# Kernel tuning notes

Measured on AMD Instinct MI355X. Metric: run time of the kernel, lower is better.

## Reference

```python
import jax, jax.numpy as jnp
import numpy as np

B, S, F = 4, 2048, 128
H, D = 4, 128          # num_heads, hidden_dim
OUT = 128              # out_features
NEG_SLOPE = 0.01       # torch leaky_relu default


def setup_inputs() -> dict:
    key = jax.random.key(0)
    ks = jax.random.split(key, 8)
    h = jax.random.normal(ks[0], (B, S, F), dtype=jnp.float32)
    # bool mask, True = masked-out key position (as used by masked_fill_)
    mask = jax.random.randint(ks[1], (B, S), 0, 2).astype(jnp.bool_)
    # Linear params (torch Linear: y = x @ W.T + b), kaiming-ish scale
    W_w = jax.random.normal(ks[2], (H * D, F), dtype=jnp.float32) / np.sqrt(F)
    W_b = jnp.zeros((H * D,), dtype=jnp.float32)
    a_w = jax.random.normal(ks[3], (1, 2 * D), dtype=jnp.float32) / np.sqrt(2 * D)
    a_b = jnp.zeros((1,), dtype=jnp.float32)
    out_w = jax.random.normal(ks[4], (OUT, H * D), dtype=jnp.float32) / np.sqrt(H * D)
    out_b = jnp.zeros((OUT,), dtype=jnp.float32)
    return {"h": h, "mask": mask, "W_w": W_w, "W_b": W_b,
            "a_w": a_w, "a_b": a_b, "out_w": out_w, "out_b": out_b}


def reference(h, mask, W_w, W_b, a_w, a_b, out_w, out_b):
    # h: [B,S,F] -> per-head projection hp: [B,H,S,D]
    hp = (h @ W_w.T + W_b).reshape(B, S, H, D).transpose(0, 2, 1, 3)
    # Additive GAT score a([h_i, h_j]) splits into two rank-1 contributions:
    # score[b,n,i,j] = leaky_relu(a1 . h_i + a2 . h_j + b)  (same math as the
    # original full [B,H,S,S,2D] concat + Linear, without materializing it).
    a1, a2 = a_w[0, :D], a_w[0, D:]
    e1 = jnp.einsum('bhsd,d->bhs', hp, a1)  # query-side term
    e2 = jnp.einsum('bhsd,d->bhs', hp, a2)  # key-side term
    scores = jax.nn.leaky_relu(e1[..., :, None] + e2[..., None, :] + a_b[0],
                               negative_slope=NEG_SLOPE)  # [B,H,S,S]
    # mask broadcast to [B,1,1,S]: masks key positions
    scores = jnp.where(mask[:, None, None, :], -jnp.inf, scores)
    attn = jax.nn.softmax(scores, axis=-1)  # [B,H,S,S]
    ctx = jnp.einsum('bhij,bhjd->bhid', attn, hp)  # [B,H,S,D]
    ctx = ctx.transpose(0, 2, 1, 3).reshape(B, S, H * D)
    out = jax.nn.relu(ctx @ out_w.T + out_b)  # [B,S,OUT]
    return out, attn
```

## Files before the change

kernel.cpp:

```cpp
#include <hip/hip_runtime.h>
#include <hip/hip_bf16.h>

#define BB 4
#define SS 2048
#define FF 128
#define DD 128
#define HD 512
#define OUTD 128
#define BH 16
#define NSL 0.01f
#define NC 258
#define NCH 128
#define CHK 16

typedef __hip_bfloat16 bf16;
typedef short bf16x8 __attribute__((ext_vector_type(8)));
typedef float f32x4 __attribute__((ext_vector_type(4)));

constexpr size_t OFF_HPF = 0;
constexpr size_t OFF_E1  = OFF_HPF + (size_t)BB*SS*HD;
constexpr size_t OFF_E2  = OFF_E1 + (size_t)BH*SS;
constexpr size_t OFF_M2  = OFF_E2 + (size_t)BH*SS;
constexpr size_t OFF_U   = OFF_M2 + 64;
constexpr size_t OFF_V   = OFF_U + (size_t)BH*SS;
constexpr size_t OFF_DS  = OFF_V + (size_t)BH*SS;
constexpr size_t OFF_SIG = OFF_DS + (size_t)BH*SS;
constexpr size_t OFF_PL  = OFF_SIG + (size_t)BH*SS;
constexpr size_t OFF_CS  = OFF_PL + (size_t)BH*2049*NC;
constexpr size_t OFF_O   = OFF_CS + (size_t)BH*NCH*NC;
constexpr size_t OFF_TOT = OFF_O + (size_t)BH*NCH*NC;
constexpr size_t OFF_CTX = OFF_TOT + (size_t)BH*NC;

__device__ inline void load8_split(const float* __restrict__ p, bf16x8& hi, bf16x8& lo) {
  f32x4 x0 = *(const f32x4*)p;
  f32x4 x1 = *(const f32x4*)(p + 4);
#pragma unroll
  for (int e = 0; e < 8; ++e) {
    float x = (e < 4) ? x0[e] : x1[e - 4];
    __hip_bfloat16 hb = __float2bfloat16(x);
    float hf = __bfloat162float(hb);
    __hip_bfloat16 lb = __float2bfloat16(x - hf);
    hi[e] = (short)__bfloat16_as_ushort(hb);
    lo[e] = (short)__bfloat16_as_ushort(lb);
  }
}

__global__ __launch_bounds__(256) void k1_hp(const float* __restrict__ h, const float* __restrict__ Ww,
                                             const float* __restrict__ Wb, float* __restrict__ hpf) {
  int wid = threadIdx.x >> 6, lane = threadIdx.x & 63;
  int tile = blockIdx.x * 4 + wid;
  int mt = tile >> 5, nt = tile & 31;
  int s0 = mt * 16, n0 = nt * 16;
  int row = lane & 15, g = lane >> 4;
  const float* pa = h  + (size_t)(s0 + row) * FF + g * 8;
  const float* pb = Ww + (size_t)(n0 + row) * FF + g * 8;
  f32x4 acc = {0.f,0.f,0.f,0.f};
#pragma unroll
  for (int ks = 0; ks < 4; ++ks) {
    bf16x8 ah, al, bh_, bl;
    load8_split(pa + ks*32, ah, al);
    load8_split(pb + ks*32, bh_, bl);
    acc = __builtin_amdgcn_mfma_f32_16x16x32_bf16(ah, bh_, acc, 0, 0, 0);
    acc = __builtin_amdgcn_mfma_f32_16x16x32_bf16(ah, bl,  acc, 0, 0, 0);
    acc = __builtin_amdgcn_mfma_f32_16x16x32_bf16(al, bh_, acc, 0, 0, 0);
  }
  int col = lane & 15;
  float bias = Wb[n0 + col];
#pragma unroll
  for (int r = 0; r < 4; ++r) {
    int orow = g*4 + r;
    hpf[(size_t)(s0 + orow) * HD + n0 + col] = acc[r] + bias;
  }
}

__global__ __launch_bounds__(256) void k2_e(const float* __restrict__ hpf, const float* __restrict__ aw,
                                            float* __restrict__ e1, float* __restrict__ e2) {
  int wid = threadIdx.x >> 6, lane = threadIdx.x & 63;
  int gw = blockIdx.x * 4 + wid;
  int bh = gw >> 11, s = gw & 2047;
  int b = bh >> 2, hh = bh & 3;
  const float* rowp = hpf + (size_t)(b*SS + s) * HD + hh * DD;
  float a1a = aw[lane],      a1b = aw[lane + 64];
  float a2a = aw[DD + lane], a2b = aw[DD + lane + 64];
  float xa = rowp[lane], xb = rowp[lane + 64];
  float r1 = xa*a1a + xb*a1b;
  float r2 = xa*a2a + xb*a2b;
  for (int o = 32; o; o >>= 1) { r1 += __shfl_down(r1, o); r2 += __shfl_down(r2, o); }
  if (lane == 0) { e1[(size_t)bh*SS + s] = r1; e2[(size_t)bh*SS + s] = r2; }
}

__global__ __launch_bounds__(256) void k2b_uv(const float* __restrict__ e2, const int* __restrict__ mask,
                                              float* __restrict__ m2out, float* __restrict__ u, float* __restrict__ v) {
  int bh = blockIdx.x; int b = bh >> 2;
  __shared__ float red[256];
  float mx = -1e30f;
  for (int j = threadIdx.x; j < SS; j += 256) {
    float val = e2[(size_t)bh*SS + j];
    if (!mask[b*SS + j]) mx = fmaxf(mx, val);
  }
  red[threadIdx.x] = mx; __syncthreads();
  for (int st = 128; st; st >>= 1) {
    if (threadIdx.x < st) red[threadIdx.x] = fmaxf(red[threadIdx.x], red[threadIdx.x + st]);
    __syncthreads();
  }
  float m2 = red[0];
  if (threadIdx.x == 0) m2out[bh] = m2;
  for (int j = threadIdx.x; j < SS; j += 256) {
    float d = e2[(size_t)bh*SS + j] - m2;
    int mk = mask[b*SS + j];
    u[(size_t)bh*SS + j] = mk ? 0.f : expf(d);
    v[(size_t)bh*SS + j] = mk ? 0.f : expf(NSL * d);
  }
}

__global__ __launch_bounds__(1024) void k2c_sort(const float* __restrict__ e2, const float* __restrict__ m2,
                                                 float* __restrict__ dso, int* __restrict__ sig) {
  int bh = blockIdx.x;
  __shared__ float val[SS];
  __shared__ int idx[SS];
  float mm = m2[bh];
  for (int j = threadIdx.x; j < SS; j += 1024) { val[j] = e2[(size_t)bh*SS + j] - mm; idx[j] = j; }
  __syncthreads();
  for (int k = 2; k <= SS; k <<= 1) {
    for (int jj = k >> 1; jj > 0; jj >>= 1) {
      for (int i = threadIdx.x; i < SS; i += 1024) {
        int l = i ^ jj;
        if (l > i) {
          bool up = ((i & k) == 0);
          float vi = val[i], vl = val[l];
          if ((vi > vl) == up) {
            val[i] = vl; val[l] = vi;
            int t = idx[i]; idx[i] = idx[l]; idx[l] = t;
          }
        }
      }
      __syncthreads();
    }
  }
  for (int j = threadIdx.x; j < SS; j += 1024) {
    dso[(size_t)bh*SS + j] = val[j];
    sig[(size_t)bh*SS + j] = idx[j];
  }
}

__global__ __launch_bounds__(320) void k3a_prefix(const float* __restrict__ hpf, const float* __restrict__ u,
                                                  const float* __restrict__ v, const int* __restrict__ sig,
                                                  float* __restrict__ PL, float* __restrict__ CS) {
  int bh = blockIdx.x >> 7;
  int ch = blockIdx.x & (NCH - 1);
  int c = threadIdx.x;
  if (c >= NC) return;
  int b = bh >> 2, hh = bh & 3;
  if (ch == 0) PL[((size_t)bh*2049 + 0)*NC + c] = 0.f;
  float acc = 0.f;
  int r0 = ch * CHK;
  for (int r = r0; r < r0 + CHK; ++r) {
    int j = sig[(size_t)bh*SS + r];
    float term;
    if (c < 128)      term = u[(size_t)bh*SS + j] * hpf[(size_t)(b*SS + j)*HD + hh*DD + c];
    else if (c < 256) term = v[(size_t)bh*SS + j] * hpf[(size_t)(b*SS + j)*HD + hh*DD + (c-128)];
    else if (c == 256) term = u[(size_t)bh*SS + j];
    else              term = v[(size_t)bh*SS + j];
    acc += term;
    PL[((size_t)bh*2049 + r + 1)*NC + c] = acc;
  }
  CS[((size_t)bh*NCH + ch)*NC + c] = acc;
}

__global__ __launch_bounds__(320) void k3b_scan(const float* __restrict__ CS, float* __restrict__ O,
                                                float* __restrict__ Tot) {
  int bh = blockIdx.x; int c = threadIdx.x;
  if (c >= NC) return;
  float acc = 0.f;
  for (int ch = 0; ch < NCH; ++ch) {
    O[((size_t)bh*NCH + ch)*NC + c] = acc;
    acc += CS[((size_t)bh*NCH + ch)*NC + c];
  }
  Tot[(size_t)bh*NC + c] = acc;
}

__global__ __launch_bounds__(256) void k4_main(const float* __restrict__ e1, const float* __restrict__ m2arr,
                                               const float* __restrict__ u, const float* __restrict__ v,
                                               const float* __restrict__ dso,
                                               const float* __restrict__ PL, const float* __restrict__ O,
                                               const float* __restrict__ Tot,
                                               const float* __restrict__ abp,
                                               float* __restrict__ ctx, float* __restrict__ attn) {
  int bh = blockIdx.x >> 6;
  int ib = blockIdx.x & 63;
  int b = bh >> 2, hh = bh & 3;
  __shared__ float ds_s[SS];
  __shared__ float u_s[SS];
  __shared__ float v_s[SS];
  for (int j = threadIdx.x; j < SS; j += 256) {
    ds_s[j] = dso[(size_t)bh*SS + j];
    u_s[j]  = u[(size_t)bh*SS + j];
    v_s[j]  = v[(size_t)bh*SS + j];
  }
  __syncthreads();
  int wid = threadIdx.x >> 6, lane = threadIdx.x & 63;
  float m2 = m2arr[bh];
  float ab = abp[0];
  const float* TotRow = Tot + (size_t)bh*NC;
  float SuT = TotRow[256];
  for (int rr = wid; rr < 32; rr += 4) {
    int i = ib*32 + rr;
    float t = e1[(size_t)bh*SS + i] + ab + m2;
    float rm = t > 0.f ? t : NSL*t;
    float alpha = expf(t - rm);
    float beta  = expf(NSL*t - rm);
    float tau = -t;
    int lo = 0, hi = SS;
    while (lo < hi) { int mid = (lo + hi) >> 1; if (ds_s[mid] < tau) lo = mid + 1; else hi = mid; }
    int r = lo;
    int ch = (r == 0) ? 0 : ((r - 1) >> 4);
    const float* PLrow = PL + ((size_t)bh*2049 + r)*NC;
    const float* Orow  = O  + ((size_t)bh*NCH + ch)*NC;
    float SU = PLrow[256] + Orow[256];
    float SV = PLrow[257] + Orow[257];
    float denom = alpha * (SuT - SU) + beta * SV;
    float inv = 1.f / denom;
    float ad = alpha * inv, bd = beta * inv;
#pragma unroll
    for (int d0 = 0; d0 < 2; ++d0) {
      int d = lane + 64*d0;
      float fu = PLrow[d]       + Orow[d];
      float fv = PLrow[128 + d] + Orow[128 + d];
      float cv = (alpha * (TotRow[d] - fu) + beta * fv) * inv;
      ctx[(size_t)(b*SS + i)*HD + hh*DD + d] = cv;
    }
    float utau = expf(tau);
    float* orow = attn + ((size_t)bh*SS + i)*SS;
#pragma unroll 2
    for (int it = 0; it < 8; ++it) {
      int j0 = it*256 + lane*4;
      f32x4 uu = *(const f32x4*)&u_s[j0];
      f32x4 vv = *(const f32x4*)&v_s[j0];
      f32x4 av;
#pragma unroll
      for (int e = 0; e < 4; ++e) av[e] = (uu[e] >= utau) ? ad*uu[e] : bd*vv[e];
      *(f32x4*)(orow + j0) = av;
    }
  }
}

__global__ __launch_bounds__(256) void k5_out(const float* __restrict__ ctx, const float* __restrict__ W2,
                                              const float* __restrict__ b2, float* __restrict__ outp) {
  int wid = threadIdx.x >> 6, lane = threadIdx.x & 63;
  int s0 = blockIdx.x * 16;
  int n0 = wid * 32;
  int row = lane & 15, g = lane >> 4;
  const float* pa  = ctx + (size_t)(s0 + row) * HD + g * 8;
  const float* pb0 = W2  + (size_t)(n0 + row) * HD + g * 8;
  const float* pb1 = W2  + (size_t)(n0 + 16 + row) * HD + g * 8;
  f32x4 acc0 = {0.f,0.f,0.f,0.f}, acc1 = {0.f,0.f,0.f,0.f};
  for (int ks = 0; ks < 16; ++ks) {
    bf16x8 ah, al, b0h, b0l, b1h, b1l;
    load8_split(pa  + ks*32, ah,  al);
    load8_split(pb0 + ks*32, b0h, b0l);
    load8_split(pb1 + ks*32, b1h, b1l);
    acc0 = __builtin_amdgcn_mfma_f32_16x16x32_bf16(ah, b0h, acc0, 0,0,0);
    acc0 = __builtin_amdgcn_mfma_f32_16x16x32_bf16(ah, b0l, acc0, 0,0,0);
    acc0 = __builtin_amdgcn_mfma_f32_16x16x32_bf16(al, b0h, acc0, 0,0,0);
    acc1 = __builtin_amdgcn_mfma_f32_16x16x32_bf16(ah, b1h, acc1, 0,0,0);
    acc1 = __builtin_amdgcn_mfma_f32_16x16x32_bf16(ah, b1l, acc1, 0,0,0);
    acc1 = __builtin_amdgcn_mfma_f32_16x16x32_bf16(al, b1h, acc1, 0,0,0);
  }
  int col = lane & 15;
  float bias0 = b2[n0 + col];
  float bias1 = b2[n0 + 16 + col];
#pragma unroll
  for (int r2 = 0; r2 < 4; ++r2) {
    int orow = g*4 + r2;
    float v0 = acc0[r2] + bias0; v0 = v0 > 0.f ? v0 : 0.f;
    float v1 = acc1[r2] + bias1; v1 = v1 > 0.f ? v1 : 0.f;
    outp[(size_t)(s0 + orow)*OUTD + n0 + col]      = v0;
    outp[(size_t)(s0 + orow)*OUTD + n0 + 16 + col] = v1;
  }
}

extern "C" void kernel_launch(void* const* d_in, const int* in_sizes, int n_in,
                              void* d_out, int out_size, void* d_ws, size_t ws_size,
                              hipStream_t stream) {
  const float* h   = (const float*)d_in[0];
  const int* mask  = (const int*)d_in[1];
  const float* Ww  = (const float*)d_in[2];
  const float* Wb  = (const float*)d_in[3];
  const float* aw  = (const float*)d_in[4];
  const float* abp = (const float*)d_in[5];
  const float* W2  = (const float*)d_in[6];
  const float* b2  = (const float*)d_in[7];
  float* ws = (float*)d_ws;
  float* hpf = ws + OFF_HPF;
  float* e1  = ws + OFF_E1;
  float* e2  = ws + OFF_E2;
  float* m2  = ws + OFF_M2;
  float* u   = ws + OFF_U;
  float* v   = ws + OFF_V;
  float* dso = ws + OFF_DS;
  int*   sig = (int*)(ws + OFF_SIG);
  float* PL  = ws + OFF_PL;
  float* CS  = ws + OFF_CS;
  float* O   = ws + OFF_O;
  float* Tot = ws + OFF_TOT;
  float* ctx = ws + OFF_CTX;
  float* outp = (float*)d_out;
  float* attn = outp + (size_t)BB*SS*OUTD;

  k1_hp<<<4096, 256, 0, stream>>>(h, Ww, Wb, hpf);
  k2_e<<<8192, 256, 0, stream>>>(hpf, aw, e1, e2);
  k2b_uv<<<16, 256, 0, stream>>>(e2, mask, m2, u, v);
  k2c_sort<<<16, 1024, 0, stream>>>(e2, m2, dso, sig);
  k3a_prefix<<<BH*NCH, 320, 0, stream>>>(hpf, u, v, sig, PL, CS);
  k3b_scan<<<16, 320, 0, stream>>>(CS, O, Tot);
  k4_main<<<BH*64, 256, 0, stream>>>(e1, m2, u, v, dso, PL, O, Tot, abp, ctx, attn);
  k5_out<<<512, 256, 0, stream>>>(ctx, W2, b2, outp);
}
```

Baseline: 440.1 us.

## Fuse max/uv with dual sort; precompute query ranks and process queries in sorted order

Merges the max/exp kernel and the sort kernel into one 1024-thread kernel. It now sorts both e2 (keys) and e1 (queries) and precomputes each query's insertion rank by binary search, so the main kernel no longer binary-searches per row. The main kernel handles rows in sorted query order, which makes neighbouring rows read nearby prefix-sum rows. It also caches Tot in shared memory and writes attn with nontemporal stores. The prefix kernel uses larger chunks with indices and weights staged in shared memory, trading fewer blocks for longer serial scans, and the query order makes ctx writes scattered.

```diff
diff --git a/kernel.cpp b/kernel.cpp
--- a/kernel.cpp
+++ b/kernel.cpp
@@ -10,26 +10,27 @@
 #define BH 16
 #define NSL 0.01f
 #define NC 258
-#define NCH 128
-#define CHK 16
+#define NCH 32
+#define CHK 64
 
 typedef __hip_bfloat16 bf16;
 typedef short bf16x8 __attribute__((ext_vector_type(8)));
 typedef float f32x4 __attribute__((ext_vector_type(4)));
 
-constexpr size_t OFF_HPF = 0;
-constexpr size_t OFF_E1  = OFF_HPF + (size_t)BB*SS*HD;
-constexpr size_t OFF_E2  = OFF_E1 + (size_t)BH*SS;
-constexpr size_t OFF_M2  = OFF_E2 + (size_t)BH*SS;
-constexpr size_t OFF_U   = OFF_M2 + 64;
-constexpr size_t OFF_V   = OFF_U + (size_t)BH*SS;
-constexpr size_t OFF_DS  = OFF_V + (size_t)BH*SS;
-constexpr size_t OFF_SIG = OFF_DS + (size_t)BH*SS;
-constexpr size_t OFF_PL  = OFF_SIG + (size_t)BH*SS;
-constexpr size_t OFF_CS  = OFF_PL + (size_t)BH*2049*NC;
-constexpr size_t OFF_O   = OFF_CS + (size_t)BH*NCH*NC;
-constexpr size_t OFF_TOT = OFF_O + (size_t)BH*NCH*NC;
-constexpr size_t OFF_CTX = OFF_TOT + (size_t)BH*NC;
+constexpr size_t OFF_HPF  = 0;
+constexpr size_t OFF_E1   = OFF_HPF + (size_t)BB*SS*HD;
+constexpr size_t OFF_E2   = OFF_E1 + (size_t)BH*SS;
+constexpr size_t OFF_M2   = OFF_E2 + (size_t)BH*SS;
+constexpr size_t OFF_U    = OFF_M2 + 64;
+constexpr size_t OFF_V    = OFF_U + (size_t)BH*SS;
+constexpr size_t OFF_SIG  = OFF_V + (size_t)BH*SS;
+constexpr size_t OFF_RHO  = OFF_SIG + (size_t)BH*SS;
+constexpr size_t OFF_RARR = OFF_RHO + (size_t)BH*SS;
+constexpr size_t OFF_PL   = OFF_RARR + (size_t)BH*SS;
+constexpr size_t OFF_CS   = OFF_PL + (size_t)BH*2049*NC;
+constexpr size_t OFF_O    = OFF_CS + (size_t)BH*NCH*NC;
+constexpr size_t OFF_TOT  = OFF_O + (size_t)BH*NCH*NC;
+constexpr size_t OFF_CTX  = OFF_TOT + (size_t)BH*NC;
 
 __device__ inline void load8_split(const float* __restrict__ p, bf16x8& hi, bf16x8& lo) {
   f32x4 x0 = *(const f32x4*)p;
@@ -89,80 +90,97 @@
   if (lane == 0) { e1[(size_t)bh*SS + s] = r1; e2[(size_t)bh*SS + s] = r2; }
 }
 
-__global__ __launch_bounds__(256) void k2b_uv(const float* __restrict__ e2, const int* __restrict__ mask,
-                                              float* __restrict__ m2out, float* __restrict__ u, float* __restrict__ v) {
+__global__ __launch_bounds__(1024) void k2bc(const float* __restrict__ e1, const float* __restrict__ e2,
+                                             const int* __restrict__ mask, const float* __restrict__ abp,
+                                             float* __restrict__ m2out, float* __restrict__ u, float* __restrict__ v,
+                                             int* __restrict__ sig, int* __restrict__ rho, int* __restrict__ rarr) {
   int bh = blockIdx.x; int b = bh >> 2;
-  __shared__ float red[256];
+  int tid = threadIdx.x;
+  __shared__ float red[1024];
+  __shared__ float va[SS]; __shared__ int ia[SS];
+  __shared__ float vb[SS]; __shared__ int ibx[SS];
   float mx = -1e30f;
-  for (int j = threadIdx.x; j < SS; j += 256) {
+  for (int j = tid; j < SS; j += 1024) {
     float val = e2[(size_t)bh*SS + j];
     if (!mask[b*SS + j]) mx = fmaxf(mx, val);
   }
-  red[threadIdx.x] = mx; __syncthreads();
-  for (int st = 128; st; st >>= 1) {
-    if (threadIdx.x < st) red[threadIdx.x] = fmaxf(red[threadIdx.x], red[threadIdx.x + st]);
+  red[tid] = mx; __syncthreads();
+  for (int st = 512; st; st >>= 1) {
+    if (tid < st) red[tid] = fmaxf(red[tid], red[tid + st]);
     __syncthreads();
   }
   float m2 = red[0];
-  if (threadIdx.x == 0) m2out[bh] = m2;
-  for (int j = threadIdx.x; j < SS; j += 256) {
-    float d = e2[(size_t)bh*SS + j] - m2;
+  if (tid == 0) m2out[bh] = m2;
+  for (int j = tid; j < SS; j += 1024) {
+    float ev = e2[(size_t)bh*SS + j];
+    float d = ev - m2;
     int mk = mask[b*SS + j];
     u[(size_t)bh*SS + j] = mk ? 0.f : expf(d);
     v[(size_t)bh*SS + j] = mk ? 0.f : expf(NSL * d);
-  }
-}
-
-__global__ __launch_bounds__(1024) void k2c_sort(const float* __restrict__ e2, const float* __restrict__ m2,
-                                                 float* __restrict__ dso, int* __restrict__ sig) {
-  int bh = blockIdx.x;
-  __shared__ float val[SS];
-  __shared__ int idx[SS];
-  float mm = m2[bh];
-  for (int j = threadIdx.x; j < SS; j += 1024) { val[j] = e2[(size_t)bh*SS + j] - mm; idx[j] = j; }
+    va[j] = ev; ia[j] = j;
+    vb[j] = e1[(size_t)bh*SS + j]; ibx[j] = j;
+  }
   __syncthreads();
+  int half = tid >> 9, t0 = tid & 511;
+  float* V = half ? vb : va;
+  int*   I = half ? ibx : ia;
   for (int k = 2; k <= SS; k <<= 1) {
     for (int jj = k >> 1; jj > 0; jj >>= 1) {
-      for (int i = threadIdx.x; i < SS; i += 1024) {
-        int l = i ^ jj;
-        if (l > i) {
-          bool up = ((i & k) == 0);
-          float vi = val[i], vl = val[l];
-          if ((vi > vl) == up) {
-            val[i] = vl; val[l] = vi;
-            int t = idx[i]; idx[i] = idx[l]; idx[l] = t;
+      for (int p = t0; p < SS; p += 512) {
+        int l = p ^ jj;
+        if (l > p) {
+          bool up = ((p & k) == 0);
+          float vp = V[p], vl = V[l];
+          if ((vp > vl) == up) {
+            V[p] = vl; V[l] = vp;
+            int t = I[p]; I[p] = I[l]; I[l] = t;
           }
         }
       }
       __syncthreads();
     }
   }
-  for (int j = threadIdx.x; j < SS; j += 1024) {
-    dso[(size_t)bh*SS + j] = val[j];
-    sig[(size_t)bh*SS + j] = idx[j];
+  float ab = abp[0];
+  for (int kk = tid; kk < SS; kk += 1024) {
+    sig[(size_t)bh*SS + kk] = ia[kk];
+    rho[(size_t)bh*SS + kk] = ibx[kk];
+    float key = -vb[kk] - ab;
+    int lo = 0, hi = SS;
+    while (lo < hi) { int mid = (lo + hi) >> 1; if (va[mid] < key) lo = mid + 1; else hi = mid; }
+    rarr[(size_t)bh*SS + kk] = lo;
   }
 }
 
 __global__ __launch_bounds__(320) void k3a_prefix(const float* __restrict__ hpf, const float* __restrict__ u,
                                                   const float* __restrict__ v, const int* __restrict__ sig,
                                                   float* __restrict__ PL, float* __restrict__ CS) {
-  int bh = blockIdx.x >> 7;
+  int bh = blockIdx.x >> 5;
   int ch = blockIdx.x & (NCH - 1);
   int c = threadIdx.x;
+  int b = bh >> 2, hh = bh & 3;
+  __shared__ int   js[CHK];
+  __shared__ float us[CHK], vs[CHK];
+  if (c < CHK) {
+    int j = sig[(size_t)bh*SS + ch*CHK + c];
+    js[c] = j;
+    us[c] = u[(size_t)bh*SS + j];
+    vs[c] = v[(size_t)bh*SS + j];
+  }
+  __syncthreads();
   if (c >= NC) return;
-  int b = bh >> 2, hh = bh & 3;
   if (ch == 0) PL[((size_t)bh*2049 + 0)*NC + c] = 0.f;
+  const float* hb = hpf + (size_t)b*SS*HD + hh*DD;
   float acc = 0.f;
-  int r0 = ch * CHK;
-  for (int r = r0; r < r0 + CHK; ++r) {
-    int j = sig[(size_t)bh*SS + r];
+  size_t plbase = ((size_t)bh*2049 + ch*CHK + 1)*NC + c;
+#pragma unroll 8
+  for (int r = 0; r < CHK; ++r) {
     float term;
-    if (c < 128)      term = u[(size_t)bh*SS + j] * hpf[(size_t)(b*SS + j)*HD + hh*DD + c];
-    else if (c < 256) term = v[(size_t)bh*SS + j] * hpf[(size_t)(b*SS + j)*HD + hh*DD + (c-128)];
-    else if (c == 256) term = u[(size_t)bh*SS + j];
-    else              term = v[(size_t)bh*SS + j];
+    if (c < 128)      term = us[r] * hb[(size_t)js[r]*HD + c];
+    else if (c < 256) term = vs[r] * hb[(size_t)js[r]*HD + (c-128)];
+    else if (c == 256) term = us[r];
+    else              term = vs[r];
     acc += term;
-    PL[((size_t)bh*2049 + r + 1)*NC + c] = acc;
+    PL[plbase + (size_t)r*NC] = acc;
   }
   CS[((size_t)bh*NCH + ch)*NC + c] = acc;
 }
@@ -181,39 +199,37 @@
 
 __global__ __launch_bounds__(256) void k4_main(const float* __restrict__ e1, const float* __restrict__ m2arr,
                                                const float* __restrict__ u, const float* __restrict__ v,
-                                               const float* __restrict__ dso,
                                                const float* __restrict__ PL, const float* __restrict__ O,
                                                const float* __restrict__ Tot,
                                                const float* __restrict__ abp,
+                                               const int* __restrict__ rho, const int* __restrict__ rarr,
                                                float* __restrict__ ctx, float* __restrict__ attn) {
   int bh = blockIdx.x >> 6;
   int ib = blockIdx.x & 63;
   int b = bh >> 2, hh = bh & 3;
-  __shared__ float ds_s[SS];
   __shared__ float u_s[SS];
   __shared__ float v_s[SS];
+  __shared__ float tot_s[NC];
   for (int j = threadIdx.x; j < SS; j += 256) {
-    ds_s[j] = dso[(size_t)bh*SS + j];
-    u_s[j]  = u[(size_t)bh*SS + j];
-    v_s[j]  = v[(size_t)bh*SS + j];
-  }
+    u_s[j] = u[(size_t)bh*SS + j];
+    v_s[j] = v[(size_t)bh*SS + j];
+  }
+  for (int c0 = threadIdx.x; c0 < NC; c0 += 256) tot_s[c0] = Tot[(size_t)bh*NC + c0];
   __syncthreads();
   int wid = threadIdx.x >> 6, lane = threadIdx.x & 63;
   float m2 = m2arr[bh];
   float ab = abp[0];
-  const float* TotRow = Tot + (size_t)bh*NC;
-  float SuT = TotRow[256];
+  float SuT = tot_s[256];
   for (int rr = wid; rr < 32; rr += 4) {
-    int i = ib*32 + rr;
+    int kk = ib*32 + rr;
+    int i = rho[(size_t)bh*SS + kk];
+    int r = rarr[(size_t)bh*SS + kk];
     float t = e1[(size_t)bh*SS + i] + ab + m2;
     float rm = t > 0.f ? t : NSL*t;
     float alpha = expf(t - rm);
     float beta  = expf(NSL*t - rm);
     float tau = -t;
-    int lo = 0, hi = SS;
-    while (lo < hi) { int mid = (lo + hi) >> 1; if (ds_s[mid] < tau) lo = mid + 1; else hi = mid; }
-    int r = lo;
-    int ch = (r == 0) ? 0 : ((r - 1) >> 4);
+    int ch = (r == 0) ? 0 : ((r - 1) >> 6);
     const float* PLrow = PL + ((size_t)bh*2049 + r)*NC;
     const float* Orow  = O  + ((size_t)bh*NCH + ch)*NC;
     float SU = PLrow[256] + Orow[256];
@@ -226,7 +242,7 @@
       int d = lane + 64*d0;
       float fu = PLrow[d]       + Orow[d];
       float fv = PLrow[128 + d] + Orow[128 + d];
-      float cv = (alpha * (TotRow[d] - fu) + beta * fv) * inv;
+      float cv = (alpha * (tot_s[d] - fu) + beta * fv) * inv;
       ctx[(size_t)(b*SS + i)*HD + hh*DD + d] = cv;
     }
     float utau = expf(tau);
@@ -239,7 +255,7 @@
       f32x4 av;
 #pragma unroll
       for (int e = 0; e < 4; ++e) av[e] = (uu[e] >= utau) ? ad*uu[e] : bd*vv[e];
-      *(f32x4*)(orow + j0) = av;
+      __builtin_nontemporal_store(av, (f32x4*)(orow + j0));
     }
   }
 }
@@ -297,8 +313,9 @@
   float* m2  = ws + OFF_M2;
   float* u   = ws + OFF_U;
   float* v   = ws + OFF_V;
-  float* dso = ws + OFF_DS;
   int*   sig = (int*)(ws + OFF_SIG);
+  int*   rho = (int*)(ws + OFF_RHO);
+  int*   rarr= (int*)(ws + OFF_RARR);
   float* PL  = ws + OFF_PL;
   float* CS  = ws + OFF_CS;
   float* O   = ws + OFF_O;
@@ -309,10 +326,9 @@
 
   k1_hp<<<4096, 256, 0, stream>>>(h, Ww, Wb, hpf);
   k2_e<<<8192, 256, 0, stream>>>(hpf, aw, e1, e2);
-  k2b_uv<<<16, 256, 0, stream>>>(e2, mask, m2, u, v);
-  k2c_sort<<<16, 1024, 0, stream>>>(e2, m2, dso, sig);
+  k2bc<<<16, 1024, 0, stream>>>(e1, e2, mask, abp, m2, u, v, sig, rho, rarr);
   k3a_prefix<<<BH*NCH, 320, 0, stream>>>(hpf, u, v, sig, PL, CS);
   k3b_scan<<<16, 320, 0, stream>>>(CS, O, Tot);
-  k4_main<<<BH*64, 256, 0, stream>>>(e1, m2, u, v, dso, PL, O, Tot, abp, ctx, attn);
+  k4_main<<<BH*64, 256, 0, stream>>>(e1, m2, u, v, PL, O, Tot, abp, rho, rarr, ctx, attn);
   k5_out<<<512, 256, 0, stream>>>(ctx, W2, b2, outp);
 }
```

After: 460.6 us. 4.7% more time.
